# Optimization experiments

Measured on AMD Instinct MI355X. Metric: run time of the kernel, lower is better.

Reference implementation:

```python
import jax, jax.numpy as jnp
import numpy as np

NUM_HEADS = 8
DIM_HEAD = 64
SCALE = DIM_HEAD * NUM_HEADS  # q *= dim_head * num_heads, as in the source


def setup_inputs() -> dict:
    key = jax.random.key(0)
    k1, k2, k3, k4 = jax.random.split(key, 4)
    B, C, H, W = 8, 64, 32, 32
    x = jax.random.normal(k1, (B, C, H, W), dtype=jnp.float32)
    # 1x1 conv == matmul over channels; small init keeps post-scale logits sane
    w_qkv = jax.random.normal(k2, (3 * NUM_HEADS * DIM_HEAD, C), dtype=jnp.float32) * 0.02
    rel_h = jax.random.normal(k3, (2 * H - 1, DIM_HEAD), dtype=jnp.float32) * 0.02
    rel_w = jax.random.normal(k4, (2 * W - 1, DIM_HEAD), dtype=jnp.float32) * 0.02
    return {"x": x, "w_qkv": w_qkv, "rel_h": rel_h, "rel_w": rel_w}


def _rel_indices(H, W):
    # flattened 2D grid positions
    pos_y = np.repeat(np.arange(H), W)  # [HW]
    pos_x = np.tile(np.arange(W), H)    # [HW]
    rel_y = pos_y[None, :] - pos_y[:, None] + (H - 1)  # [HW, HW] in [0, 2H-2]
    rel_x = pos_x[None, :] - pos_x[:, None] + (W - 1)  # [HW, HW] in [0, 2W-2]
    return jnp.asarray(rel_y), jnp.asarray(rel_x)


def reference(x, w_qkv, rel_h, rel_w):
    B, C, H, W = x.shape
    n = H * W
    # 1x1 conv (bias=False) -> per-pixel matmul
    xf = x.reshape(B, C, n)                              # b c n
    qkv = jnp.einsum('oc,bcn->bon', w_qkv, xf)           # b (3 h d) n
    q, k, v = jnp.split(qkv, 3, axis=1)
    def to_heads(t):  # b (h d) n -> b h n d
        return t.reshape(B, NUM_HEADS, DIM_HEAD, n).transpose(0, 1, 3, 2)
    q, k, v = to_heads(q), to_heads(k), to_heads(v)
    q = q * SCALE  # scale applied before QK^T AND before pos bias (in-place in torch)

    sim = jnp.einsum('bhid,bhjd->bhij', q, k)            # [B, h, n, n]

    # relative position bias: q_i . rel_h[dy] + q_i . rel_w[dx]
    logits_h = jnp.einsum('bhid,rd->bhir', q, rel_h)     # [B, h, n, 2H-1]
    logits_w = jnp.einsum('bhid,rd->bhir', q, rel_w)     # [B, h, n, 2W-1]
    rel_y, rel_x = _rel_indices(H, W)                    # [n, n] each
    i_idx = jnp.arange(n)[:, None]                       # [n, 1]
    bias = logits_h[:, :, i_idx, rel_y] + logits_w[:, :, i_idx, rel_x]  # [B,h,n,n]

    attn = jax.nn.softmax(sim + bias, axis=-1)
    out = jnp.einsum('bhij,bhjd->bhid', attn, v)         # [B, h, n, d]
    out = out.transpose(0, 1, 3, 2).reshape(B, NUM_HEADS * DIM_HEAD, H, W)
    return out
```

## Files before the change

kernel.cpp:

```cpp
#include <hip/hip_runtime.h>
#include <hip/hip_bf16.h>
#include <hip/hip_fp16.h>

typedef _Float16 h8 __attribute__((ext_vector_type(8)));
typedef _Float16 h2 __attribute__((ext_vector_type(2)));
typedef unsigned short us8 __attribute__((ext_vector_type(8)));
typedef float f4 __attribute__((ext_vector_type(4)));

#define NH 8
#define DH 64
#define NPIX 1024
#define CIN 64
#define NBH 64
#define QSCALE (512.0f * 1.44269504f)
#define LOSCALE 2048.0f
#define INV_LOSCALE (1.0f / 2048.0f)
#define DTHR 12.0f

__device__ __forceinline__ void gload_lds16(const void* g, void* lds) {
  __builtin_amdgcn_global_load_lds(
      (const __attribute__((address_space(1))) void*)g,
      (__attribute__((address_space(3))) void*)lds, 16, 0, 0);
}

__device__ __forceinline__ float fexp2(float x) {
#if __has_builtin(__builtin_amdgcn_exp2f)
  return __builtin_amdgcn_exp2f(x);
#else
  return exp2f(x);
#endif
}

__device__ __forceinline__ unsigned pk16(float a, float b) {
  auto r = __builtin_amdgcn_cvt_pkrtz(a, b);
  union { decltype(r) h; unsigned u; } x;
  x.h = r;
  return x.u;
}

__device__ __forceinline__ f4 max4(f4 a, f4 b) {
  f4 r;
  r[0] = fmaxf(a[0], b[0]); r[1] = fmaxf(a[1], b[1]);
  r[2] = fmaxf(a[2], b[2]); r[3] = fmaxf(a[3], b[3]);
  return r;
}

__global__ __launch_bounds__(256) void qkv_mfma(
    const float* __restrict__ x, const float* __restrict__ wqkv,
    _Float16* __restrict__ Qh, _Float16* __restrict__ Ql,
    _Float16* __restrict__ Kh, _Float16* __restrict__ Kl,
    _Float16* __restrict__ Vv) {
  __shared__ __align__(16) char QS[49152];
  char* Wh = QS;
  char* Wl = QS + 16384;
  char* Xh = QS + 32768;
  char* Xl = QS + 40960;

  const int tid = threadIdx.x;
  const int lane = tid & 63;
  const int w = tid >> 6;
  const int c = lane & 15;
  const int g = lane >> 4;
  const int o0 = blockIdx.x * 128;
  const int p0 = blockIdx.y * 64;
  const int b = blockIdx.z;

  #pragma unroll
  for (int it = 0; it < 4; ++it) {
    int task = tid + it * 256;
    int oct = task & 7, o = task >> 3;
    const f4* wr = (const f4*)(wqkv + (size_t)(o0 + o) * CIN + oct * 8);
    f4 wa = wr[0], wb = wr[1];
    h8 hi, lo;
    #pragma unroll
    for (int e = 0; e < 8; ++e) {
      float v = e < 4 ? wa[e] : wb[e - 4];
      _Float16 h = (_Float16)v;
      hi[e] = h;
      lo[e] = (_Float16)((v - (float)h) * LOSCALE);
    }
    int byo = o * 128 + ((oct ^ (o & 7)) << 4);
    *(h8*)(Wh + byo) = hi;
    *(h8*)(Wl + byo) = lo;
  }
  {
    int kp = tid & 31;
    int pgrp = tid >> 5;
    const float* xr0 = x + ((size_t)b * CIN + 2 * kp) * NPIX + p0 + pgrp * 8;
    const float* xr1 = xr0 + NPIX;
    f4 a0 = *(const f4*)xr0, a1 = *(const f4*)(xr0 + 4);
    f4 b0 = *(const f4*)xr1, b1 = *(const f4*)(xr1 + 4);
    int oct = kp >> 2;
    int slot4 = (kp & 3) * 4;
    #pragma unroll
    for (int e = 0; e < 8; ++e) {
      float v0 = e < 4 ? a0[e] : a1[e - 4];
      float v1 = e < 4 ? b0[e] : b1[e - 4];
      _Float16 h0 = (_Float16)v0, h1 = (_Float16)v1;
      float l0f = (v0 - (float)h0) * LOSCALE;
      float l1f = (v1 - (float)h1) * LOSCALE;
      int p = pgrp * 8 + e;
      int byo = p * 128 + ((oct ^ (p & 7)) << 4) + slot4;
      union { h2 h; unsigned u; } uh, ul;
      uh.h[0] = h0; uh.h[1] = h1;
      ul.h[0] = (_Float16)l0f; ul.h[1] = (_Float16)l1f;
      *(unsigned*)(Xh + byo) = uh.u;
      *(unsigned*)(Xl + byo) = ul.u;
    }
  }
  __syncthreads();

  f4 zf = {0.f, 0.f, 0.f, 0.f};
  f4 acc[2][4], cor[2][4];
  #pragma unroll
  for (int oi = 0; oi < 2; ++oi)
    #pragma unroll
    for (int pi = 0; pi < 4; ++pi) { acc[oi][pi] = zf; cor[oi][pi] = zf; }

  const int ob = w * 32;
  #pragma unroll
  for (int kh = 0; kh < 2; ++kh) {
    h8 ah[2], al[2], bh[4], bl[4];
    #pragma unroll
    for (int oi = 0; oi < 2; ++oi) {
      int orow = ob + ((c >> 2) << 3) + (c & 3) + oi * 4;
      int ch = (((kh * 4 + g) ^ (orow & 7)) << 4);
      ah[oi] = *(const h8*)(Wh + orow * 128 + ch);
      al[oi] = *(const h8*)(Wl + orow * 128 + ch);
    }
    #pragma unroll
    for (int pi = 0; pi < 4; ++pi) {
      int prow = pi * 16 + c;
      int ch = (((kh * 4 + g) ^ (prow & 7)) << 4);
      bh[pi] = *(const h8*)(Xh + prow * 128 + ch);
      bl[pi] = *(const h8*)(Xl + prow * 128 + ch);
    }
    __builtin_amdgcn_s_setprio(1);
    #pragma unroll
    for (int oi = 0; oi < 2; ++oi)
      #pragma unroll
      for (int pi = 0; pi < 4; ++pi) {
        acc[oi][pi] = __builtin_amdgcn_mfma_f32_16x16x32_f16(ah[oi], bh[pi], acc[oi][pi], 0, 0, 0);
        cor[oi][pi] = __builtin_amdgcn_mfma_f32_16x16x32_f16(ah[oi], bl[pi], cor[oi][pi], 0, 0, 0);
        cor[oi][pi] = __builtin_amdgcn_mfma_f32_16x16x32_f16(al[oi], bh[pi], cor[oi][pi], 0, 0, 0);
      }
    __builtin_amdgcn_s_setprio(0);
  }

  const int part = o0 >> 9;
  const float scl = part == 0 ? QSCALE : 1.0f;
  _Float16* dsth = part == 0 ? Qh : (part == 1 ? Kh : Vv);
  _Float16* dstl = part == 0 ? Ql : (part == 1 ? Kl : nullptr);
  #pragma unroll
  for (int pi = 0; pi < 4; ++pi) {
    int obase = o0 + ob + 8 * g;
    int h = (obase >> 6) & 7;
    int d = obase & 63;
    int p_abs = p0 + pi * 16 + c;
    size_t off = (((size_t)(b * NH + h)) * NPIX + p_abs) * DH + d;
    h8 hv, lv;
    #pragma unroll
    for (int oi = 0; oi < 2; ++oi)
      #pragma unroll
      for (int reg = 0; reg < 4; ++reg) {
        float v = (acc[oi][pi][reg] + cor[oi][pi][reg] * INV_LOSCALE) * scl;
        _Float16 hh = (_Float16)v;
        hv[oi * 4 + reg] = hh;
        lv[oi * 4 + reg] = (_Float16)((v - (float)hh) * LOSCALE);
      }
    *(h8*)(dsth + off) = hv;
    if (dstl) *(h8*)(dstl + off) = lv;
  }
}

__global__ __launch_bounds__(256, 2) void attn_mfma(
    const _Float16* __restrict__ Qh, const _Float16* __restrict__ Ql,
    const _Float16* __restrict__ Kh, const _Float16* __restrict__ Kl,
    const _Float16* __restrict__ V,
    const float* __restrict__ rel_h, const float* __restrict__ rel_w,
    float* __restrict__ out) {
  __shared__ __align__(16) char SMem[65536];
  char* SP = SMem + 49152;
  _Float16* LHc = (_Float16*)(SMem + 57344);
  _Float16* LWT = (_Float16*)(SMem + 32768);
  float* OT = (float*)SMem;

  const int tid = threadIdx.x;
  const int lane = tid & 63;
  const int w = tid >> 6;
  const int wu = __builtin_amdgcn_readfirstlane(w);
  const int c = lane & 15;
  const int g = lane >> 4;
  const int bx = blockIdx.x;
  const int bh = ((bx & 7) << 3) | ((bx >> 3) & 7);
  const int i0 = (bx >> 6) << 7;
  const int swz = (c & 7) << 4;

  const _Float16* Qhg = Qh + (size_t)bh * NPIX * DH;
  const _Float16* Qlg = Ql + (size_t)bh * NPIX * DH;
  const _Float16* Khg = Kh + (size_t)bh * NPIX * DH;
  const _Float16* Klg = Kl + (size_t)bh * NPIX * DH;
  const _Float16* Vg  = V  + (size_t)bh * NPIX * DH;

  const h8* Qr0h = (const h8*)(Qhg + (size_t)(i0 + w * 32 + c) * DH);
  const h8* Qr0l = (const h8*)(Qlg + (size_t)(i0 + w * 32 + c) * DH);
  const h8* Qr1h = (const h8*)(Qhg + (size_t)(i0 + w * 32 + 16 + c) * DH);
  const h8* Qr1l = (const h8*)(Qlg + (size_t)(i0 + w * 32 + 16 + c) * DH);
  h8 q0h[2] = {Qr0h[g], Qr0h[4 + g]};
  h8 q0l[2] = {Qr0l[g], Qr0l[4 + g]};
  h8 q1h[2] = {Qr1h[g], Qr1h[4 + g]};
  h8 q1l[2] = {Qr1l[g], Qr1l[4 + g]};

  const int s0i = wu * 128 + lane;
  const int s1i = s0i + 64;
  const int ko0 = (s0i >> 3) * 128 + (((s0i & 7) ^ ((s0i >> 3) & 7)) << 4);
  const int ko1 = (s1i >> 3) * 128 + (((s1i & 7) ^ ((s1i >> 3) & 7)) << 4);

  #pragma unroll
  for (int it = 0; it < 2; ++it) {
    int task = tid + it * 256;
    int oct = task & 7, s = task >> 3;
    int ss = s < 63 ? s : 62;
    const float* sh = rel_h + (size_t)ss * DH + oct * 8;
    const float* sw = rel_w + (size_t)ss * DH + oct * 8;
    h8 hh, ww;
    #pragma unroll
    for (int e = 0; e < 8; ++e) {
      hh[e] = (_Float16)sh[e];
      ww[e] = (_Float16)sw[e];
    }
    int byo = s * 128 + ((oct ^ (s & 7)) << 4);
    *(h8*)(SMem + byo) = hh;
    *(h8*)(SMem + 16384 + byo) = ww;
  }
  __syncthreads();

  const int yi = (i0 + w * 32) >> 5;
  f4 zf = {0.f, 0.f, 0.f, 0.f};
  #pragma unroll
  for (int rs = 0; rs < 2; ++rs) {
    f4 lhD[4], lwD[4], lhDc[4], lwDc[4];
    #pragma unroll
    for (int st = 0; st < 4; ++st) { lhD[st] = zf; lwD[st] = zf; lhDc[st] = zf; lwDc[st] = zf; }
    #pragma unroll
    for (int kh = 0; kh < 2; ++kh) {
      h8 bq = rs ? q1h[kh] : q0h[kh];
      h8 bl = rs ? q1l[kh] : q0l[kh];
      #pragma unroll
      for (int st = 0; st < 4; ++st) {
        int srow = st * 16 + c;
        int chb = srow * 128 + (((kh * 4 + g) ^ (srow & 7)) << 4);
        h8 ra = *(const h8*)(SMem + chb);
        h8 wa = *(const h8*)(SMem + 16384 + chb);
        lhD[st]  = __builtin_amdgcn_mfma_f32_16x16x32_f16(ra, bq, lhD[st], 0, 0, 0);
        lhDc[st] = __builtin_amdgcn_mfma_f32_16x16x32_f16(ra, bl, lhDc[st], 0, 0, 0);
        lwD[st]  = __builtin_amdgcn_mfma_f32_16x16x32_f16(wa, bq, lwD[st], 0, 0, 0);
        lwDc[st] = __builtin_amdgcn_mfma_f32_16x16x32_f16(wa, bl, lwDc[st], 0, 0, 0);
      }
    }
    int lrow = w * 32 + rs * 16 + c;
    #pragma unroll
    for (int st = 0; st < 4; ++st)
      #pragma unroll
      for (int reg = 0; reg < 4; ++reg) {
        int s = st * 16 + 4 * g + reg;
        float lhv = lhD[st][reg] + lhDc[st][reg] * INV_LOSCALE;
        float lwv = lwD[st][reg] + lwDc[st][reg] * INV_LOSCALE;
        int k = s - 31 + yi;
        if (k >= 0 && k < 32) LHc[k * 128 + lrow] = (_Float16)lhv;
        LWT[lrow * 64 + s] = (_Float16)lwv;
      }
  }
  __syncthreads();

  h8 lwp0, lwp1;
  #pragma unroll
  for (int jbp = 0; jbp < 2; ++jbp)
    #pragma unroll
    for (int reg = 0; reg < 4; ++reg) {
      lwp0[jbp * 4 + reg] = LWT[(w * 32 + c) * 64 + 31 + jbp * 16 + 4 * g + reg - c];
      lwp1[jbp * 4 + reg] = LWT[(w * 32 + 16 + c) * 64 + 31 + jbp * 16 + 4 * g + reg - 16 - c];
    }
  __syncthreads();

  {
    gload_lds16((const char*)Khg + ko0, SMem + wu * 2048);
    gload_lds16((const char*)Khg + ko1, SMem + wu * 2048 + 1024);
    gload_lds16((const char*)Klg + ko0, SMem + 16384 + wu * 2048);
    gload_lds16((const char*)Klg + ko1, SMem + 16384 + wu * 2048 + 1024);
    int jp = tid & 31, dd = tid >> 5;
    const h8* vr = (const h8*)(Vg + (size_t)(2 * jp) * DH);
    h8 v0 = vr[dd], v1 = vr[8 + dd];
    us8 u0 = *(const us8*)&v0, u1 = *(const us8*)&v1;
    #pragma unroll
    for (int e = 0; e < 8; ++e) {
      int d = dd * 8 + e;
      unsigned int val = (unsigned int)u0[e] | ((unsigned int)u1[e] << 16);
      *(unsigned int*)(SMem + 32768 + d * 128 + (((jp >> 2) ^ (d & 7)) << 4) + (jp & 3) * 4) = val;
    }
  }
  __syncthreads();

  float m0 = -1e30f, m1 = -1e30f, lp0 = 0.f, lp1 = 0.f;
  f4 o0_[4], o1_[4];
  #pragma unroll
  for (int dt = 0; dt < 4; ++dt) { o0_[dt] = zf; o1_[dt] = zf; }

  int cur = 0;
  #pragma unroll 1
  for (int t = 0; t < 16; ++t) {
    char* Kc  = SMem + cur * 8192;
    char* KLc = SMem + 16384 + cur * 8192;
    char* Vc  = SMem + 32768 + cur * 8192;
    const int nxt = cur ^ 1;
    const bool pre = t < 15;
    const int jp = tid & 31, dd = tid >> 5;
    h8 v0 = {}, v1 = {};
    if (pre) {
      const char* kg  = (const char*)Khg + (size_t)(t + 1) * 8192;
      const char* klg = (const char*)Klg + (size_t)(t + 1) * 8192;
      gload_lds16(kg + ko0, SMem + nxt * 8192 + wu * 2048);
      gload_lds16(kg + ko1, SMem + nxt * 8192 + wu * 2048 + 1024);
      gload_lds16(klg + ko0, SMem + 16384 + nxt * 8192 + wu * 2048);
      gload_lds16(klg + ko1, SMem + 16384 + nxt * 8192 + wu * 2048 + 1024);
      const h8* vr = (const h8*)(Vg + (size_t)((t + 1) * 64 + 2 * jp) * DH);
      v0 = vr[dd];
      v1 = vr[8 + dd];
    }

    f4 s0[4], c0[4], s1[4], c1[4];
    #pragma unroll
    for (int jb = 0; jb < 4; ++jb) { s0[jb] = zf; c0[jb] = zf; s1[jb] = zf; c1[jb] = zf; }
    #pragma unroll
    for (int kh = 0; kh < 2; ++kh) {
      h8 b0h = q0h[kh], b0l = q0l[kh], b1h = q1h[kh], b1l = q1l[kh];
      #pragma unroll
      for (int jb = 0; jb < 4; ++jb) {
        int jrow = jb * 16 + c;
        int chb = jrow * 128 + (((kh * 4 + g) ^ (c & 7)) << 4);
        h8 ah = *(const h8*)(Kc + chb);
        h8 al = *(const h8*)(KLc + chb);
        __builtin_amdgcn_s_setprio(1);
        s0[jb] = __builtin_amdgcn_mfma_f32_16x16x32_f16(ah, b0h, s0[jb], 0, 0, 0);
        c0[jb] = __builtin_amdgcn_mfma_f32_16x16x32_f16(al, b0h, c0[jb], 0, 0, 0);
        c0[jb] = __builtin_amdgcn_mfma_f32_16x16x32_f16(ah, b0l, c0[jb], 0, 0, 0);
        s1[jb] = __builtin_amdgcn_mfma_f32_16x16x32_f16(ah, b1h, s1[jb], 0, 0, 0);
        c1[jb] = __builtin_amdgcn_mfma_f32_16x16x32_f16(al, b1h, c1[jb], 0, 0, 0);
        c1[jb] = __builtin_amdgcn_mfma_f32_16x16x32_f16(ah, b1l, c1[jb], 0, 0, 0);
        __builtin_amdgcn_s_setprio(0);
      }
    }

    auto finish = [&](f4* s_, f4* c_, const h8& lwp, float& m_s, float& lp,
                      f4* o_, int rs) {
      int rr = w * 32 + rs * 16 + c;
      float lh01[2] = {(float)LHc[(2 * t) * 128 + rr],
                       (float)LHc[(2 * t + 1) * 128 + rr]};
      #pragma unroll
      for (int jb = 0; jb < 4; ++jb)
        #pragma unroll
        for (int reg = 0; reg < 4; ++reg)
          s_[jb][reg] += c_[jb][reg] * INV_LOSCALE +
                         (float)lwp[(jb & 1) * 4 + reg] + lh01[jb >> 1];
      f4 ab = max4(s_[0], s_[1]);
      f4 cd = max4(s_[2], s_[3]);
      f4 ef = max4(ab, cd);
      float mx = fmaxf(fmaxf(ef[0], ef[1]), fmaxf(ef[2], ef[3]));
      mx = fmaxf(mx, __shfl_xor(mx, 16, 64));
      mx = fmaxf(mx, __shfl_xor(mx, 32, 64));
      bool sk = mx <= m_s + DTHR;
      if (!__all(sk)) {
        float mn = fmaxf(m_s, mx);
        float corr = fexp2(m_s - mn);
        m_s = mn;
        lp *= corr;
        #pragma unroll
        for (int dt = 0; dt < 4; ++dt)
          #pragma unroll
          for (int reg = 0; reg < 4; ++reg)
            o_[dt][reg] *= corr;
      }
      float sum = 0.f;
      char* pbse = SP + w * 2048 + c * 128;
      #pragma unroll
      for (int jb = 0; jb < 4; ++jb) {
        f4 p;
        #pragma unroll
        for (int reg = 0; reg < 4; ++reg) {
          p[reg] = fexp2(s_[jb][reg] - m_s);
          sum += p[reg];
        }
        unsigned long long u = (unsigned long long)pk16(p[0], p[1]) |
                               ((unsigned long long)pk16(p[2], p[3]) << 32);
        *(unsigned long long*)(pbse + ((jb * 32 + 8 * g) ^ swz)) = u;
      }
      lp += sum;
    };

    finish(s0, c0, lwp0, m0, lp0, o0_, 0);
    __builtin_amdgcn_wave_barrier();

    h8 vbr[2][4];
    #pragma unroll
    for (int kh = 0; kh < 2; ++kh) {
      int och = ((kh * 4 + g) ^ (c & 7)) << 4;
      h8 pb = *(const h8*)(SP + w * 2048 + c * 128 + och);
      __builtin_amdgcn_s_setprio(1);
      #pragma unroll
      for (int dt = 0; dt < 4; ++dt) {
        vbr[kh][dt] = *(const h8*)(Vc + (dt * 16 + c) * 128 + och);
        o0_[dt] = __builtin_amdgcn_mfma_f32_16x16x32_f16(vbr[kh][dt], pb, o0_[dt], 0, 0, 0);
      }
      __builtin_amdgcn_s_setprio(0);
    }

    finish(s1, c1, lwp1, m1, lp1, o1_, 1);
    __builtin_amdgcn_wave_barrier();

    #pragma unroll
    for (int kh = 0; kh < 2; ++kh) {
      int och = ((kh * 4 + g) ^ (c & 7)) << 4;
      h8 pb = *(const h8*)(SP + w * 2048 + c * 128 + och);
      __builtin_amdgcn_s_setprio(1);
      #pragma unroll
      for (int dt = 0; dt < 4; ++dt)
        o1_[dt] = __builtin_amdgcn_mfma_f32_16x16x32_f16(vbr[kh][dt], pb, o1_[dt], 0, 0, 0);
      __builtin_amdgcn_s_setprio(0);
    }

    if (pre) {
      us8 u0 = *(const us8*)&v0, u1 = *(const us8*)&v1;
      char* Vn = SMem + 32768 + nxt * 8192;
      #pragma unroll
      for (int e = 0; e < 8; ++e) {
        int d = dd * 8 + e;
        unsigned int val = (unsigned int)u0[e] | ((unsigned int)u1[e] << 16);
        *(unsigned int*)(Vn + d * 128 + (((jp >> 2) ^ (d & 7)) << 4) + (jp & 3) * 4) = val;
      }
    }
    __syncthreads();
    cur = nxt;
  }

  float a0 = lp0;
  a0 += __shfl_xor(a0, 16, 64);
  a0 += __shfl_xor(a0, 32, 64);
  float r0 = __builtin_amdgcn_rcpf(a0);
  float a1 = lp1;
  a1 += __shfl_xor(a1, 16, 64);
  a1 += __shfl_xor(a1, 32, 64);
  float r1 = __builtin_amdgcn_rcpf(a1);
  #pragma unroll
  for (int dt = 0; dt < 4; ++dt)
    #pragma unroll
    for (int reg = 0; reg < 4; ++reg) {
      int d = dt * 16 + 4 * g + reg;
      int sw = (d & 7) << 3;
      int il0 = w * 32 + c;
      OT[d * 128 + (il0 ^ sw)] = o0_[dt][reg] * r0;
      OT[d * 128 + ((il0 + 16) ^ sw)] = o1_[dt][reg] * r1;
    }
  __syncthreads();
  #pragma unroll
  for (int it = 0; it < 8; ++it) {
    int task = tid + it * 256;
    int rq = task & 31, d = task >> 5;
    f4 vv = *(const f4*)&OT[d * 128 + ((rq * 4) ^ ((d & 7) << 3))];
    *(f4*)(out + (((size_t)bh * 64 + d) << 10) + i0 + rq * 4) = vv;
  }
}

extern "C" void kernel_launch(void* const* d_in, const int* in_sizes, int n_in,
                              void* d_out, int out_size, void* d_ws, size_t ws_size,
                              hipStream_t stream) {
  const float* x  = (const float*)d_in[0];
  const float* wq = (const float*)d_in[1];
  const float* rh = (const float*)d_in[2];
  const float* rw = (const float*)d_in[3];
  float* out = (float*)d_out;

  const size_t sz = (size_t)NBH * NPIX * DH;
  _Float16* Qh = (_Float16*)d_ws;
  _Float16* Ql = Qh + sz;
  _Float16* Kh = Ql + sz;
  _Float16* Kl = Kh + sz;
  _Float16* V  = Kl + sz;

  qkv_mfma<<<dim3(12, 16, 8), 256, 0, stream>>>(x, wq, Qh, Ql, Kh, Kl, V);
  attn_mfma<<<dim3(512), 256, 0, stream>>>(Qh, Ql, Kh, Kl, V, rh, rw, out);
}
```

Baseline: 77.92 us.

## Split KV range across two wave groups per block with flash-decoding style merge

Doubles the block to 512 threads, with two groups of four waves that each process half of the key/value sequence in a single-buffered loop. The partial softmax states are merged through LDS at the end. The low-part correction terms now accumulate directly into the main accumulators, since the lo values are stored unscaled, which drops the separate correction MFMA accumulators and the INV_LOSCALE fixups. The intent is more parallelism per query tile and lower register pressure. The cost is the loss of double buffering, extra block-wide barriers each iteration, and possible fp16 underflow in the unscaled low parts.

Result: slower. 211.0 us (+170.8%).

```diff
diff --git a/kernel.cpp b/kernel.cpp
--- a/kernel.cpp
+++ b/kernel.cpp
@@ -166,29 +166,25 @@
         float v = (acc[oi][pi][reg] + cor[oi][pi][reg] * INV_LOSCALE) * scl;
         _Float16 hh = (_Float16)v;
         hv[oi * 4 + reg] = hh;
-        lv[oi * 4 + reg] = (_Float16)((v - (float)hh) * LOSCALE);
+        lv[oi * 4 + reg] = (_Float16)(v - (float)hh);
       }
     *(h8*)(dsth + off) = hv;
     if (dstl) *(h8*)(dstl + off) = lv;
   }
 }
 
-__global__ __launch_bounds__(256, 2) void attn_mfma(
+__global__ __launch_bounds__(512, 4) void attn_mfma(
     const _Float16* __restrict__ Qh, const _Float16* __restrict__ Ql,
     const _Float16* __restrict__ Kh, const _Float16* __restrict__ Kl,
     const _Float16* __restrict__ V,
     const float* __restrict__ rel_h, const float* __restrict__ rel_w,
     float* __restrict__ out) {
-  __shared__ __align__(16) char SMem[65536];
-  char* SP = SMem + 49152;
-  _Float16* LHc = (_Float16*)(SMem + 57344);
-  _Float16* LWT = (_Float16*)(SMem + 32768);
-  float* OT = (float*)SMem;
-
+  __shared__ __align__(16) char SMem[73728];
   const int tid = threadIdx.x;
   const int lane = tid & 63;
-  const int w = tid >> 6;
-  const int wu = __builtin_amdgcn_readfirstlane(w);
+  const int wu = tid >> 6;
+  const int lw = wu & 3;
+  const int grp = wu >> 2;
   const int c = lane & 15;
   const int g = lane >> 4;
   const int bx = blockIdx.x;
@@ -196,30 +192,37 @@
   const int i0 = (bx >> 6) << 7;
   const int swz = (c & 7) << 4;
 
+  char* KHb = SMem + grp * 8192;
+  char* KLb = SMem + 16384 + grp * 8192;
+  char* VBb = SMem + 32768 + grp * 8192;
+  char* SPw = SMem + 49152 + wu * 2048;
+  _Float16* LHc = (_Float16*)(SMem + 65536);
+  _Float16* LWT = (_Float16*)(SMem + 32768);
+
   const _Float16* Qhg = Qh + (size_t)bh * NPIX * DH;
   const _Float16* Qlg = Ql + (size_t)bh * NPIX * DH;
   const _Float16* Khg = Kh + (size_t)bh * NPIX * DH;
   const _Float16* Klg = Kl + (size_t)bh * NPIX * DH;
   const _Float16* Vg  = V  + (size_t)bh * NPIX * DH;
 
-  const h8* Qr0h = (const h8*)(Qhg + (size_t)(i0 + w * 32 + c) * DH);
-  const h8* Qr0l = (const h8*)(Qlg + (size_t)(i0 + w * 32 + c) * DH);
-  const h8* Qr1h = (const h8*)(Qhg + (size_t)(i0 + w * 32 + 16 + c) * DH);
-  const h8* Qr1l = (const h8*)(Qlg + (size_t)(i0 + w * 32 + 16 + c) * DH);
+  const h8* Qr0h = (const h8*)(Qhg + (size_t)(i0 + lw * 32 + c) * DH);
+  const h8* Qr0l = (const h8*)(Qlg + (size_t)(i0 + lw * 32 + c) * DH);
+  const h8* Qr1h = (const h8*)(Qhg + (size_t)(i0 + lw * 32 + 16 + c) * DH);
+  const h8* Qr1l = (const h8*)(Qlg + (size_t)(i0 + lw * 32 + 16 + c) * DH);
   h8 q0h[2] = {Qr0h[g], Qr0h[4 + g]};
   h8 q0l[2] = {Qr0l[g], Qr0l[4 + g]};
   h8 q1h[2] = {Qr1h[g], Qr1h[4 + g]};
   h8 q1l[2] = {Qr1l[g], Qr1l[4 + g]};
 
-  const int s0i = wu * 128 + lane;
+  const int s0i = lw * 128 + lane;
   const int s1i = s0i + 64;
   const int ko0 = (s0i >> 3) * 128 + (((s0i & 7) ^ ((s0i >> 3) & 7)) << 4);
   const int ko1 = (s1i >> 3) * 128 + (((s1i & 7) ^ ((s1i >> 3) & 7)) << 4);
-
-  #pragma unroll
-  for (int it = 0; it < 2; ++it) {
-    int task = tid + it * 256;
-    int oct = task & 7, s = task >> 3;
+  const int ltid = tid & 255;
+  const int jp = ltid & 31, dd = ltid >> 5;
+
+  {
+    int oct = tid & 7, s = tid >> 3;
     int ss = s < 63 ? s : 62;
     const float* sh = rel_h + (size_t)ss * DH + oct * 8;
     const float* sw = rel_w + (size_t)ss * DH + oct * 8;
@@ -235,13 +238,13 @@
   }
   __syncthreads();
 
-  const int yi = (i0 + w * 32) >> 5;
+  const int yi = (i0 + lw * 32) >> 5;
   f4 zf = {0.f, 0.f, 0.f, 0.f};
   #pragma unroll
   for (int rs = 0; rs < 2; ++rs) {
-    f4 lhD[4], lwD[4], lhDc[4], lwDc[4];
-    #pragma unroll
-    for (int st = 0; st < 4; ++st) { lhD[st] = zf; lwD[st] = zf; lhDc[st] = zf; lwDc[st] = zf; }
+    f4 lhD[4], lwD[4];
+    #pragma unroll
+    for (int st = 0; st < 4; ++st) { lhD[st] = zf; lwD[st] = zf; }
     #pragma unroll
     for (int kh = 0; kh < 2; ++kh) {
       h8 bq = rs ? q1h[kh] : q0h[kh];
@@ -252,51 +255,49 @@
         int chb = srow * 128 + (((kh * 4 + g) ^ (srow & 7)) << 4);
         h8 ra = *(const h8*)(SMem + chb);
         h8 wa = *(const h8*)(SMem + 16384 + chb);
-        lhD[st]  = __builtin_amdgcn_mfma_f32_16x16x32_f16(ra, bq, lhD[st], 0, 0, 0);
-        lhDc[st] = __builtin_amdgcn_mfma_f32_16x16x32_f16(ra, bl, lhDc[st], 0, 0, 0);
-        lwD[st]  = __builtin_amdgcn_mfma_f32_16x16x32_f16(wa, bq, lwD[st], 0, 0, 0);
-        lwDc[st] = __builtin_amdgcn_mfma_f32_16x16x32_f16(wa, bl, lwDc[st], 0, 0, 0);
-      }
-    }
-    int lrow = w * 32 + rs * 16 + c;
+        lhD[st] = __builtin_amdgcn_mfma_f32_16x16x32_f16(ra, bq, lhD[st], 0, 0, 0);
+        lhD[st] = __builtin_amdgcn_mfma_f32_16x16x32_f16(ra, bl, lhD[st], 0, 0, 0);
+        lwD[st] = __builtin_amdgcn_mfma_f32_16x16x32_f16(wa, bq, lwD[st], 0, 0, 0);
+        lwD[st] = __builtin_amdgcn_mfma_f32_16x16x32_f16(wa, bl, lwD[st], 0, 0, 0);
+      }
+    }
+    int lrow = lw * 32 + rs * 16 + c;
     #pragma unroll
     for (int st = 0; st < 4; ++st)
       #pragma unroll
       for (int reg = 0; reg < 4; ++reg) {
         int s = st * 16 + 4 * g + reg;
-        float lhv = lhD[st][reg] + lhDc[st][reg] * INV_LOSCALE;
-        float lwv = lwD[st][reg] + lwDc[st][reg] * INV_LOSCALE;
         int k = s - 31 + yi;
-        if (k >= 0 && k < 32) LHc[k * 128 + lrow] = (_Float16)lhv;
-        LWT[lrow * 64 + s] = (_Float16)lwv;
-      }
-  }
-  __syncthreads();
-
-  h8 lwp0, lwp1;
+        if (k >= 0 && k < 32) LHc[k * 128 + lrow] = (_Float16)lhD[st][reg];
+        LWT[lrow * 64 + s] = (_Float16)lwD[st][reg];
+      }
+  }
+  __syncthreads();
+
+  float lwp0[8], lwp1[8];
   #pragma unroll
   for (int jbp = 0; jbp < 2; ++jbp)
     #pragma unroll
     for (int reg = 0; reg < 4; ++reg) {
-      lwp0[jbp * 4 + reg] = LWT[(w * 32 + c) * 64 + 31 + jbp * 16 + 4 * g + reg - c];
-      lwp1[jbp * 4 + reg] = LWT[(w * 32 + 16 + c) * 64 + 31 + jbp * 16 + 4 * g + reg - 16 - c];
+      lwp0[jbp * 4 + reg] = (float)LWT[(lw * 32 + c) * 64 + 31 + jbp * 16 + 4 * g + reg - c];
+      lwp1[jbp * 4 + reg] = (float)LWT[(lw * 32 + 16 + c) * 64 + 31 + jbp * 16 + 4 * g + reg - 16 - c];
     }
   __syncthreads();
 
   {
-    gload_lds16((const char*)Khg + ko0, SMem + wu * 2048);
-    gload_lds16((const char*)Khg + ko1, SMem + wu * 2048 + 1024);
-    gload_lds16((const char*)Klg + ko0, SMem + 16384 + wu * 2048);
-    gload_lds16((const char*)Klg + ko1, SMem + 16384 + wu * 2048 + 1024);
-    int jp = tid & 31, dd = tid >> 5;
-    const h8* vr = (const h8*)(Vg + (size_t)(2 * jp) * DH);
+    const int tg0 = grp << 3;
+    gload_lds16((const char*)Khg + tg0 * 8192 + ko0, KHb + lw * 2048);
+    gload_lds16((const char*)Khg + tg0 * 8192 + ko1, KHb + lw * 2048 + 1024);
+    gload_lds16((const char*)Klg + tg0 * 8192 + ko0, KLb + lw * 2048);
+    gload_lds16((const char*)Klg + tg0 * 8192 + ko1, KLb + lw * 2048 + 1024);
+    const h8* vr = (const h8*)(Vg + (size_t)(tg0 * 64 + 2 * jp) * DH);
     h8 v0 = vr[dd], v1 = vr[8 + dd];
     us8 u0 = *(const us8*)&v0, u1 = *(const us8*)&v1;
     #pragma unroll
     for (int e = 0; e < 8; ++e) {
       int d = dd * 8 + e;
       unsigned int val = (unsigned int)u0[e] | ((unsigned int)u1[e] << 16);
-      *(unsigned int*)(SMem + 32768 + d * 128 + (((jp >> 2) ^ (d & 7)) << 4) + (jp & 3) * 4) = val;
+      *(unsigned int*)(VBb + d * 128 + (((jp >> 2) ^ (d & 7)) << 4) + (jp & 3) * 4) = val;
     }
   }
   __syncthreads();
@@ -306,65 +307,52 @@
   #pragma unroll
   for (int dt = 0; dt < 4; ++dt) { o0_[dt] = zf; o1_[dt] = zf; }
 
-  int cur = 0;
   #pragma unroll 1
-  for (int t = 0; t < 16; ++t) {
-    char* Kc  = SMem + cur * 8192;
-    char* KLc = SMem + 16384 + cur * 8192;
-    char* Vc  = SMem + 32768 + cur * 8192;
-    const int nxt = cur ^ 1;
-    const bool pre = t < 15;
-    const int jp = tid & 31, dd = tid >> 5;
-    h8 v0 = {}, v1 = {};
+  for (int t = 0; t < 8; ++t) {
+    const int tg = (grp << 3) + t;
+    const bool pre = t < 7;
+    h8 v0n = {}, v1n = {};
     if (pre) {
-      const char* kg  = (const char*)Khg + (size_t)(t + 1) * 8192;
-      const char* klg = (const char*)Klg + (size_t)(t + 1) * 8192;
-      gload_lds16(kg + ko0, SMem + nxt * 8192 + wu * 2048);
-      gload_lds16(kg + ko1, SMem + nxt * 8192 + wu * 2048 + 1024);
-      gload_lds16(klg + ko0, SMem + 16384 + nxt * 8192 + wu * 2048);
-      gload_lds16(klg + ko1, SMem + 16384 + nxt * 8192 + wu * 2048 + 1024);
-      const h8* vr = (const h8*)(Vg + (size_t)((t + 1) * 64 + 2 * jp) * DH);
-      v0 = vr[dd];
-      v1 = vr[8 + dd];
-    }
-
-    f4 s0[4], c0[4], s1[4], c1[4];
-    #pragma unroll
-    for (int jb = 0; jb < 4; ++jb) { s0[jb] = zf; c0[jb] = zf; s1[jb] = zf; c1[jb] = zf; }
+      const h8* vr = (const h8*)(Vg + (size_t)((tg + 1) * 64 + 2 * jp) * DH);
+      v0n = vr[dd];
+      v1n = vr[8 + dd];
+    }
+
+    f4 s0[4], s1[4];
+    #pragma unroll
+    for (int jb = 0; jb < 4; ++jb) { s0[jb] = zf; s1[jb] = zf; }
     #pragma unroll
     for (int kh = 0; kh < 2; ++kh) {
       h8 b0h = q0h[kh], b0l = q0l[kh], b1h = q1h[kh], b1l = q1l[kh];
       #pragma unroll
       for (int jb = 0; jb < 4; ++jb) {
-        int jrow = jb * 16 + c;
-        int chb = jrow * 128 + (((kh * 4 + g) ^ (c & 7)) << 4);
-        h8 ah = *(const h8*)(Kc + chb);
-        h8 al = *(const h8*)(KLc + chb);
+        int chb = (jb * 16 + c) * 128 + (((kh * 4 + g) ^ (c & 7)) << 4);
+        h8 ah = *(const h8*)(KHb + chb);
+        h8 al = *(const h8*)(KLb + chb);
         __builtin_amdgcn_s_setprio(1);
         s0[jb] = __builtin_amdgcn_mfma_f32_16x16x32_f16(ah, b0h, s0[jb], 0, 0, 0);
-        c0[jb] = __builtin_amdgcn_mfma_f32_16x16x32_f16(al, b0h, c0[jb], 0, 0, 0);
-        c0[jb] = __builtin_amdgcn_mfma_f32_16x16x32_f16(ah, b0l, c0[jb], 0, 0, 0);
+        s0[jb] = __builtin_amdgcn_mfma_f32_16x16x32_f16(al, b0h, s0[jb], 0, 0, 0);
+        s0[jb] = __builtin_amdgcn_mfma_f32_16x16x32_f16(ah, b0l, s0[jb], 0, 0, 0);
         s1[jb] = __builtin_amdgcn_mfma_f32_16x16x32_f16(ah, b1h, s1[jb], 0, 0, 0);
-        c1[jb] = __builtin_amdgcn_mfma_f32_16x16x32_f16(al, b1h, c1[jb], 0, 0, 0);
-        c1[jb] = __builtin_amdgcn_mfma_f32_16x16x32_f16(ah, b1l, c1[jb], 0, 0, 0);
+        s1[jb] = __builtin_amdgcn_mfma_f32_16x16x32_f16(al, b1h, s1[jb], 0, 0, 0);
+        s1[jb] = __builtin_amdgcn_mfma_f32_16x16x32_f16(ah, b1l, s1[jb], 0, 0, 0);
         __builtin_amdgcn_s_setprio(0);
       }
     }
 
-    auto finish = [&](f4* s_, f4* c_, const h8& lwp, float& m_s, float& lp,
+    auto finish = [&](f4* s_, const float* lwp, float& m_s, float& lp,
                       f4* o_, int rs) {
-      int rr = w * 32 + rs * 16 + c;
-      float lh01[2] = {(float)LHc[(2 * t) * 128 + rr],
-                       (float)LHc[(2 * t + 1) * 128 + rr]};
-      #pragma unroll
-      for (int jb = 0; jb < 4; ++jb)
+      int rr = lw * 32 + rs * 16 + c;
+      float lh0 = (float)LHc[(2 * tg) * 128 + rr];
+      float lh1 = (float)LHc[(2 * tg + 1) * 128 + rr];
+      #pragma unroll
+      for (int jb = 0; jb < 4; ++jb) {
+        float lhv = (jb >> 1) ? lh1 : lh0;
         #pragma unroll
         for (int reg = 0; reg < 4; ++reg)
-          s_[jb][reg] += c_[jb][reg] * INV_LOSCALE +
-                         (float)lwp[(jb & 1) * 4 + reg] + lh01[jb >> 1];
-      f4 ab = max4(s_[0], s_[1]);
-      f4 cd = max4(s_[2], s_[3]);
-      f4 ef = max4(ab, cd);
+          s_[jb][reg] += lwp[(jb & 1) * 4 + reg] + lhv;
+      }
+      f4 ef = max4(max4(s_[0], s_[1]), max4(s_[2], s_[3]));
       float mx = fmaxf(fmaxf(ef[0], ef[1]), fmaxf(ef[2], ef[3]));
       mx = fmaxf(mx, __shfl_xor(mx, 16, 64));
       mx = fmaxf(mx, __shfl_xor(mx, 32, 64));
@@ -381,7 +369,7 @@
             o_[dt][reg] *= corr;
       }
       float sum = 0.f;
-      char* pbse = SP + w * 2048 + c * 128;
+      char* pbse = SPw + c * 128;
       #pragma unroll
       for (int jb = 0; jb < 4; ++jb) {
         f4 p;
@@ -397,30 +385,36 @@
       lp += sum;
     };
 
-    finish(s0, c0, lwp0, m0, lp0, o0_, 0);
-    __builtin_amdgcn_wave_barrier();
+    finish(s0, lwp0, m0, lp0, o0_, 0);
+    __syncthreads();
+    if (pre) {
+      gload_lds16((const char*)Khg + (tg + 1) * 8192 + ko0, KHb + lw * 2048);
+      gload_lds16((const char*)Khg + (tg + 1) * 8192 + ko1, KHb + lw * 2048 + 1024);
+      gload_lds16((const char*)Klg + (tg + 1) * 8192 + ko0, KLb + lw * 2048);
+      gload_lds16((const char*)Klg + (tg + 1) * 8192 + ko1, KLb + lw * 2048 + 1024);
+    }
 
     h8 vbr[2][4];
     #pragma unroll
     for (int kh = 0; kh < 2; ++kh) {
       int och = ((kh * 4 + g) ^ (c & 7)) << 4;
-      h8 pb = *(const h8*)(SP + w * 2048 + c * 128 + och);
+      h8 pb = *(const h8*)(SPw + c * 128 + och);
       __builtin_amdgcn_s_setprio(1);
       #pragma unroll
       for (int dt = 0; dt < 4; ++dt) {
-        vbr[kh][dt] = *(const h8*)(Vc + (dt * 16 + c) * 128 + och);
+        vbr[kh][dt] = *(const h8*)(VBb + (dt * 16 + c) * 128 + och);
         o0_[dt] = __builtin_amdgcn_mfma_f32_16x16x32_f16(vbr[kh][dt], pb, o0_[dt], 0, 0, 0);
       }
       __builtin_amdgcn_s_setprio(0);
     }
 
-    finish(s1, c1, lwp1, m1, lp1, o1_, 1);
+    finish(s1, lwp1, m1, lp1, o1_, 1);
     __builtin_amdgcn_wave_barrier();
 
     #pragma unroll
     for (int kh = 0; kh < 2; ++kh) {
       int och = ((kh * 4 + g) ^ (c & 7)) << 4;
-      h8 pb = *(const h8*)(SP + w * 2048 + c * 128 + och);
+      h8 pb = *(const h8*)(SPw + c * 128 + och);
       __builtin_amdgcn_s_setprio(1);
       #pragma unroll
       for (int dt = 0; dt < 4; ++dt)
@@ -428,42 +422,74 @@
       __builtin_amdgcn_s_setprio(0);
     }
 
+    __syncthreads();
     if (pre) {
-      us8 u0 = *(const us8*)&v0, u1 = *(const us8*)&v1;
-      char* Vn = SMem + 32768 + nxt * 8192;
+      us8 u0 = *(const us8*)&v0n, u1 = *(const us8*)&v1n;
       #pragma unroll
       for (int e = 0; e < 8; ++e) {
         int d = dd * 8 + e;
         unsigned int val = (unsigned int)u0[e] | ((unsigned int)u1[e] << 16);
-        *(unsigned int*)(Vn + d * 128 + (((jp >> 2) ^ (d & 7)) << 4) + (jp & 3) * 4) = val;
-      }
-    }
-    __syncthreads();
-    cur = nxt;
-  }
-
-  float a0 = lp0;
-  a0 += __shfl_xor(a0, 16, 64);
-  a0 += __shfl_xor(a0, 32, 64);
-  float r0 = __builtin_amdgcn_rcpf(a0);
-  float a1 = lp1;
-  a1 += __shfl_xor(a1, 16, 64);
-  a1 += __shfl_xor(a1, 32, 64);
-  float r1 = __builtin_amdgcn_rcpf(a1);
-  #pragma unroll
-  for (int dt = 0; dt < 4; ++dt)
+        *(unsigned int*)(VBb + d * 128 + (((jp >> 2) ^ (d & 7)) << 4) + (jp & 3) * 4) = val;
+      }
+    }
+  }
+
+  __syncthreads();
+  {
+    float* exw = (float*)SMem + ((size_t)wu * 64 + lane) * 21;
+    exw[0] = m0; exw[1] = lp0; exw[2] = m1; exw[3] = lp1;
+    int wb = grp ? 0 : 2;
+    #pragma unroll
+    for (int k = 0; k < 2; ++k)
+      #pragma unroll
+      for (int reg = 0; reg < 4; ++reg) {
+        exw[4 + k * 4 + reg] = o0_[wb + k][reg];
+        exw[12 + k * 4 + reg] = o1_[wb + k][reg];
+      }
+  }
+  __syncthreads();
+  float r0, r1;
+  f4 om0[2], om1[2];
+  const int mybase = grp * 2;
+  {
+    const float* exp_ = (const float*)SMem + ((size_t)(wu ^ 4) * 64 + lane) * 21;
+    float pm0 = exp_[0], plp0 = exp_[1], pm1 = exp_[2], plp1 = exp_[3];
+    float M0 = fmaxf(m0, pm0);
+    float ca0 = fexp2(m0 - M0), cb0 = fexp2(pm0 - M0);
+    float M1 = fmaxf(m1, pm1);
+    float ca1 = fexp2(m1 - M1), cb1 = fexp2(pm1 - M1);
+    float L0 = lp0 * ca0 + plp0 * cb0;
+    float L1 = lp1 * ca1 + plp1 * cb1;
+    L0 += __shfl_xor(L0, 16, 64);
+    L0 += __shfl_xor(L0, 32, 64);
+    L1 += __shfl_xor(L1, 16, 64);
+    L1 += __shfl_xor(L1, 32, 64);
+    r0 = __builtin_amdgcn_rcpf(L0);
+    r1 = __builtin_amdgcn_rcpf(L1);
+    #pragma unroll
+    for (int k = 0; k < 2; ++k)
+      #pragma unroll
+      for (int reg = 0; reg < 4; ++reg) {
+        om0[k][reg] = o0_[mybase + k][reg] * ca0 + exp_[4 + k * 4 + reg] * cb0;
+        om1[k][reg] = o1_[mybase + k][reg] * ca1 + exp_[12 + k * 4 + reg] * cb1;
+      }
+  }
+  __syncthreads();
+  float* OT = (float*)SMem;
+  #pragma unroll
+  for (int k = 0; k < 2; ++k)
     #pragma unroll
     for (int reg = 0; reg < 4; ++reg) {
-      int d = dt * 16 + 4 * g + reg;
+      int d = (mybase + k) * 16 + 4 * g + reg;
       int sw = (d & 7) << 3;
-      int il0 = w * 32 + c;
-      OT[d * 128 + (il0 ^ sw)] = o0_[dt][reg] * r0;
-      OT[d * 128 + ((il0 + 16) ^ sw)] = o1_[dt][reg] * r1;
-    }
-  __syncthreads();
-  #pragma unroll
-  for (int it = 0; it < 8; ++it) {
-    int task = tid + it * 256;
+      int il0 = lw * 32 + c;
+      OT[d * 128 + (il0 ^ sw)] = om0[k][reg] * r0;
+      OT[d * 128 + ((il0 + 16) ^ sw)] = om1[k][reg] * r1;
+    }
+  __syncthreads();
+  #pragma unroll
+  for (int it = 0; it < 4; ++it) {
+    int task = tid + it * 512;
     int rq = task & 31, d = task >> 5;
     f4 vv = *(const f4*)&OT[d * 128 + ((rq * 4) ^ ((d & 7) << 3))];
     *(f4*)(out + (((size_t)bh * 64 + d) << 10) + i0 + rq * 4) = vv;
@@ -487,5 +513,5 @@
   _Float16* V  = Kl + sz;
 
   qkv_mfma<<<dim3(12, 16, 8), 256, 0, stream>>>(x, wq, Qh, Ql, Kh, Kl, V);
-  attn_mfma<<<dim3(512), 256, 0, stream>>>(Qh, Ql, Kh, Kl, V, rh, rw, out);
-}
+  attn_mfma<<<dim3(512), 512, 0, stream>>>(Qh, Ql, Kh, Kl, V, rh, rw, out);
+}
```

## Accumulate low-part correction MFMAs into the main accumulator, drop LOSCALE scaling

Applied to the files above, without the earlier changes.

Stores the fp16 low residual of Q/K without the 2048 prescale, so the correction MFMAs can accumulate directly into the main score accumulators. This removes the separate correction accumulators and their per-element fused multiply-add, which lowers register pressure and VALU work in the softmax finish step. It also changes the LHc layout so the two row-bias values load as one packed h2, keeps the width-bias values as preconverted floats, and splits the exp sum into four partial sums. The risk is precision loss, since unscaled fp16 residuals can underflow into subnormals or zero.

Result: no change. 78.85 us (+1.2%).

```diff
diff --git a/kernel.cpp b/kernel.cpp
--- a/kernel.cpp
+++ b/kernel.cpp
@@ -166,7 +166,7 @@
         float v = (acc[oi][pi][reg] + cor[oi][pi][reg] * INV_LOSCALE) * scl;
         _Float16 hh = (_Float16)v;
         hv[oi * 4 + reg] = hh;
-        lv[oi * 4 + reg] = (_Float16)((v - (float)hh) * LOSCALE);
+        lv[oi * 4 + reg] = (_Float16)(v - (float)hh);
       }
     *(h8*)(dsth + off) = hv;
     if (dstl) *(h8*)(dstl + off) = lv;
@@ -239,9 +239,9 @@
   f4 zf = {0.f, 0.f, 0.f, 0.f};
   #pragma unroll
   for (int rs = 0; rs < 2; ++rs) {
-    f4 lhD[4], lwD[4], lhDc[4], lwDc[4];
-    #pragma unroll
-    for (int st = 0; st < 4; ++st) { lhD[st] = zf; lwD[st] = zf; lhDc[st] = zf; lwDc[st] = zf; }
+    f4 lhD[4], lwD[4];
+    #pragma unroll
+    for (int st = 0; st < 4; ++st) { lhD[st] = zf; lwD[st] = zf; }
     #pragma unroll
     for (int kh = 0; kh < 2; ++kh) {
       h8 bq = rs ? q1h[kh] : q0h[kh];
@@ -252,10 +252,10 @@
         int chb = srow * 128 + (((kh * 4 + g) ^ (srow & 7)) << 4);
         h8 ra = *(const h8*)(SMem + chb);
         h8 wa = *(const h8*)(SMem + 16384 + chb);
-        lhD[st]  = __builtin_amdgcn_mfma_f32_16x16x32_f16(ra, bq, lhD[st], 0, 0, 0);
-        lhDc[st] = __builtin_amdgcn_mfma_f32_16x16x32_f16(ra, bl, lhDc[st], 0, 0, 0);
-        lwD[st]  = __builtin_amdgcn_mfma_f32_16x16x32_f16(wa, bq, lwD[st], 0, 0, 0);
-        lwDc[st] = __builtin_amdgcn_mfma_f32_16x16x32_f16(wa, bl, lwDc[st], 0, 0, 0);
+        lhD[st] = __builtin_amdgcn_mfma_f32_16x16x32_f16(ra, bq, lhD[st], 0, 0, 0);
+        lhD[st] = __builtin_amdgcn_mfma_f32_16x16x32_f16(ra, bl, lhD[st], 0, 0, 0);
+        lwD[st] = __builtin_amdgcn_mfma_f32_16x16x32_f16(wa, bq, lwD[st], 0, 0, 0);
+        lwD[st] = __builtin_amdgcn_mfma_f32_16x16x32_f16(wa, bl, lwD[st], 0, 0, 0);
       }
     }
     int lrow = w * 32 + rs * 16 + c;
@@ -264,22 +264,21 @@
       #pragma unroll
       for (int reg = 0; reg < 4; ++reg) {
         int s = st * 16 + 4 * g + reg;
-        float lhv = lhD[st][reg] + lhDc[st][reg] * INV_LOSCALE;
-        float lwv = lwD[st][reg] + lwDc[st][reg] * INV_LOSCALE;
         int k = s - 31 + yi;
-        if (k >= 0 && k < 32) LHc[k * 128 + lrow] = (_Float16)lhv;
-        LWT[lrow * 64 + s] = (_Float16)lwv;
-      }
-  }
-  __syncthreads();
-
-  h8 lwp0, lwp1;
+        if (k >= 0 && k < 32)
+          LHc[(k >> 1) * 256 + lrow * 2 + (k & 1)] = (_Float16)lhD[st][reg];
+        LWT[lrow * 64 + s] = (_Float16)lwD[st][reg];
+      }
+  }
+  __syncthreads();
+
+  float lwp0[8], lwp1[8];
   #pragma unroll
   for (int jbp = 0; jbp < 2; ++jbp)
     #pragma unroll
     for (int reg = 0; reg < 4; ++reg) {
-      lwp0[jbp * 4 + reg] = LWT[(w * 32 + c) * 64 + 31 + jbp * 16 + 4 * g + reg - c];
-      lwp1[jbp * 4 + reg] = LWT[(w * 32 + 16 + c) * 64 + 31 + jbp * 16 + 4 * g + reg - 16 - c];
+      lwp0[jbp * 4 + reg] = (float)LWT[(w * 32 + c) * 64 + 31 + jbp * 16 + 4 * g + reg - c];
+      lwp1[jbp * 4 + reg] = (float)LWT[(w * 32 + 16 + c) * 64 + 31 + jbp * 16 + 4 * g + reg - 16 - c];
     }
   __syncthreads();
 
@@ -328,43 +327,41 @@
       v1 = vr[8 + dd];
     }
 
-    f4 s0[4], c0[4], s1[4], c1[4];
-    #pragma unroll
-    for (int jb = 0; jb < 4; ++jb) { s0[jb] = zf; c0[jb] = zf; s1[jb] = zf; c1[jb] = zf; }
+    f4 s0[4], s1[4];
+    #pragma unroll
+    for (int jb = 0; jb < 4; ++jb) { s0[jb] = zf; s1[jb] = zf; }
     #pragma unroll
     for (int kh = 0; kh < 2; ++kh) {
       h8 b0h = q0h[kh], b0l = q0l[kh], b1h = q1h[kh], b1l = q1l[kh];
       #pragma unroll
       for (int jb = 0; jb < 4; ++jb) {
-        int jrow = jb * 16 + c;
-        int chb = jrow * 128 + (((kh * 4 + g) ^ (c & 7)) << 4);
+        int chb = (jb * 16 + c) * 128 + (((kh * 4 + g) ^ (c & 7)) << 4);
         h8 ah = *(const h8*)(Kc + chb);
         h8 al = *(const h8*)(KLc + chb);
         __builtin_amdgcn_s_setprio(1);
         s0[jb] = __builtin_amdgcn_mfma_f32_16x16x32_f16(ah, b0h, s0[jb], 0, 0, 0);
-        c0[jb] = __builtin_amdgcn_mfma_f32_16x16x32_f16(al, b0h, c0[jb], 0, 0, 0);
-        c0[jb] = __builtin_amdgcn_mfma_f32_16x16x32_f16(ah, b0l, c0[jb], 0, 0, 0);
+        s0[jb] = __builtin_amdgcn_mfma_f32_16x16x32_f16(al, b0h, s0[jb], 0, 0, 0);
+        s0[jb] = __builtin_amdgcn_mfma_f32_16x16x32_f16(ah, b0l, s0[jb], 0, 0, 0);
         s1[jb] = __builtin_amdgcn_mfma_f32_16x16x32_f16(ah, b1h, s1[jb], 0, 0, 0);
-        c1[jb] = __builtin_amdgcn_mfma_f32_16x16x32_f16(al, b1h, c1[jb], 0, 0, 0);
-        c1[jb] = __builtin_amdgcn_mfma_f32_16x16x32_f16(ah, b1l, c1[jb], 0, 0, 0);
+        s1[jb] = __builtin_amdgcn_mfma_f32_16x16x32_f16(al, b1h, s1[jb], 0, 0, 0);
+        s1[jb] = __builtin_amdgcn_mfma_f32_16x16x32_f16(ah, b1l, s1[jb], 0, 0, 0);
         __builtin_amdgcn_s_setprio(0);
       }
     }
 
-    auto finish = [&](f4* s_, f4* c_, const h8& lwp, float& m_s, float& lp,
+    auto finish = [&](f4* s_, const float* lwp, float& m_s, float& lp,
                       f4* o_, int rs) {
       int rr = w * 32 + rs * 16 + c;
-      float lh01[2] = {(float)LHc[(2 * t) * 128 + rr],
-                       (float)LHc[(2 * t + 1) * 128 + rr]};
-      #pragma unroll
-      for (int jb = 0; jb < 4; ++jb)
+      h2 lhu = *(const h2*)(LHc + t * 256 + rr * 2);
+      float lh0 = (float)lhu[0], lh1 = (float)lhu[1];
+      #pragma unroll
+      for (int jb = 0; jb < 4; ++jb) {
+        float lhv = (jb >> 1) ? lh1 : lh0;
         #pragma unroll
         for (int reg = 0; reg < 4; ++reg)
-          s_[jb][reg] += c_[jb][reg] * INV_LOSCALE +
-                         (float)lwp[(jb & 1) * 4 + reg] + lh01[jb >> 1];
-      f4 ab = max4(s_[0], s_[1]);
-      f4 cd = max4(s_[2], s_[3]);
-      f4 ef = max4(ab, cd);
+          s_[jb][reg] += lwp[(jb & 1) * 4 + reg] + lhv;
+      }
+      f4 ef = max4(max4(s_[0], s_[1]), max4(s_[2], s_[3]));
       float mx = fmaxf(fmaxf(ef[0], ef[1]), fmaxf(ef[2], ef[3]));
       mx = fmaxf(mx, __shfl_xor(mx, 16, 64));
       mx = fmaxf(mx, __shfl_xor(mx, 32, 64));
@@ -380,24 +377,22 @@
           for (int reg = 0; reg < 4; ++reg)
             o_[dt][reg] *= corr;
       }
-      float sum = 0.f;
+      f4 psum = zf;
       char* pbse = SP + w * 2048 + c * 128;
       #pragma unroll
       for (int jb = 0; jb < 4; ++jb) {
         f4 p;
         #pragma unroll
-        for (int reg = 0; reg < 4; ++reg) {
-          p[reg] = fexp2(s_[jb][reg] - m_s);
-          sum += p[reg];
-        }
+        for (int reg = 0; reg < 4; ++reg) p[reg] = fexp2(s_[jb][reg] - m_s);
+        psum[0] += p[0]; psum[1] += p[1]; psum[2] += p[2]; psum[3] += p[3];
         unsigned long long u = (unsigned long long)pk16(p[0], p[1]) |
                                ((unsigned long long)pk16(p[2], p[3]) << 32);
         *(unsigned long long*)(pbse + ((jb * 32 + 8 * g) ^ swz)) = u;
       }
-      lp += sum;
+      lp += (psum[0] + psum[1]) + (psum[2] + psum[3]);
     };
 
-    finish(s0, c0, lwp0, m0, lp0, o0_, 0);
+    finish(s0, lwp0, m0, lp0, o0_, 0);
     __builtin_amdgcn_wave_barrier();
 
     h8 vbr[2][4];
@@ -414,7 +409,7 @@
       __builtin_amdgcn_s_setprio(0);
     }
 
-    finish(s1, c1, lwp1, m1, lp1, o1_, 1);
+    finish(s1, lwp1, m1, lp1, o1_, 1);
     __builtin_amdgcn_wave_barrier();
 
     #pragma unroll
```
